# Optimization experiments

Hardware: AMD Instinct MI355X
Metric: run time of the kernel (lower is better)

## Reference

```python
import jax, jax.numpy as jnp
import numpy as np
import math

# Poincare ball, curvature c=1 (fixed, requires_grad=False in source)
C = 1.0
SQC = math.sqrt(C)
EPS = 1e-15
BALL_EPS = 1e-5  # projection margin onto the open ball


def _beta(n):
    # B(n/2, 1/2) -- beta-concatenation scale from HNN++ (Shimizu et al.)
    return math.exp(math.lgamma(n / 2.0) + math.lgamma(0.5) - math.lgamma((n + 1) / 2.0))


def _project(x, axis):
    max_norm = (1.0 - BALL_EPS) / SQC
    n = jnp.linalg.norm(x, axis=axis, keepdims=True)
    return x * jnp.minimum(1.0, max_norm / jnp.maximum(n, EPS))


def _expmap0(v, axis):
    n = jnp.maximum(jnp.linalg.norm(v, axis=axis, keepdims=True), EPS)
    return _project(jnp.tanh(SQC * n) * v / (SQC * n), axis)


def _logmap0(x, axis):
    n = jnp.maximum(jnp.linalg.norm(x, axis=axis, keepdims=True), EPS)
    sn = jnp.minimum(SQC * n, 1.0 - 1e-7)
    return jnp.arctanh(sn) * x / (SQC * n)


def _hrelu(x, axis):
    # HReLU: relu in the tangent space at the origin
    return _expmap0(jax.nn.relu(_logmap0(x, axis)), axis)


def _poincare_fc(x, z, r):
    # Poincare fully-connected layer (HNN++): x [..., d_in], z [d_in, d_out], r [d_out]
    zn = jnp.maximum(jnp.linalg.norm(z, axis=0), EPS)        # [d_out]
    zu = z / zn                                               # unit columns
    cx2 = C * jnp.sum(x * x, axis=-1, keepdims=True)          # c*||x||^2
    drcr = 2.0 * SQC * r                                      # [d_out]
    # unidirectional Poincare MLR
    v = (2.0 * zn / SQC) * jnp.arcsinh(
        (2.0 * SQC * (x @ zu) * jnp.cosh(drcr) - (1.0 + cx2) * jnp.sinh(drcr))
        / jnp.maximum(1.0 - cx2, EPS)
    )
    # map generalized coordinates back onto the ball
    y = jnp.sinh(SQC * v) / SQC
    y = y / (1.0 + jnp.sqrt(1.0 + C * jnp.sum(y * y, axis=-1, keepdims=True)))
    return _project(y, -1)


def _hconv(x, z, r, k):
    # HConvolution2d: beta-concat unfold of kxk patches (man_dim = channels), then Poincare FC
    B, Cin, H, W = x.shape
    oh, ow = H - k + 1, W - k + 1
    v = _logmap0(x, axis=1) * (_beta(Cin * k * k) / _beta(Cin))
    # torch.F.unfold ordering: feature index = c*k*k + i*k + j
    patches = jnp.stack([v[:, :, i:i + oh, j:j + ow] for i in range(k) for j in range(k)], axis=2)
    p = patches.reshape(B, Cin * k * k, oh * ow)
    xp = _expmap0(p, axis=1).transpose(0, 2, 1)   # [B, L, Cin*k*k]
    out = _poincare_fc(xp, z, r)                  # [B, L, Cout]
    return out.transpose(0, 2, 1).reshape(B, -1, oh, ow)


def _hmaxpool2(x):
    # HMaxPool2d(kernel=2, stride=2): pick the patch element with max distance to origin
    # (distance is monotonic in the norm, so argmax over channel norm suffices)
    B, Cc, H, W = x.shape
    h, w = H // 2, W // 2
    xb = x.reshape(B, Cc, h, 2, w, 2).transpose(0, 2, 4, 1, 3, 5).reshape(B, h, w, Cc, 4)
    nb = jnp.sum(xb * xb, axis=3)                 # [B, h, w, 4] squared norms
    idx = jnp.argmax(nb, axis=-1)                 # [B, h, w]
    out = jnp.take_along_axis(xb, idx[..., None, None], axis=-1)[..., 0]  # [B, h, w, Cc]
    return out.transpose(0, 3, 1, 2)


def _hflatten(x):
    # ManifoldTensor.flatten(start_dim=1): beta-concatenation flatten (man_dim 1 -> last)
    B, Cin = x.shape[0], x.shape[1]
    n = x.shape[1] * x.shape[2] * x.shape[3]
    v = _logmap0(x, axis=1) * (_beta(n) / _beta(Cin))
    return _expmap0(v.reshape(B, n), axis=-1)


def setup_inputs() -> dict:
    key = jax.random.key(0)
    ks = jax.random.split(key, 12)
    B = 1024
    s = 0.05
    x = _expmap0(0.1 * jax.random.normal(ks[0], (B, 3, 32, 32), jnp.float32), axis=1)
    return {
        "x": x,
        "z1": s * jax.random.normal(ks[1], (75, 6), jnp.float32),    # 3*5*5 -> 6
        "b1": s * jax.random.normal(ks[2], (6,), jnp.float32),
        "z2": s * jax.random.normal(ks[3], (150, 16), jnp.float32),  # 6*5*5 -> 16
        "b2": s * jax.random.normal(ks[4], (16,), jnp.float32),
        "zf1": s * jax.random.normal(ks[5], (400, 120), jnp.float32),
        "bf1": s * jax.random.normal(ks[6], (120,), jnp.float32),
        "zf2": s * jax.random.normal(ks[7], (120, 84), jnp.float32),
        "bf2": s * jax.random.normal(ks[8], (84,), jnp.float32),
        "zf3": s * jax.random.normal(ks[9], (84, 10), jnp.float32),
        "bf3": s * jax.random.normal(ks[10], (10,), jnp.float32),
    }


def reference(x, z1, b1, z2, b2, zf1, bf1, zf2, bf2, zf3, bf3):
    h = _hmaxpool2(_hrelu(_hconv(x, z1, b1, 5), axis=1))    # [B,6,14,14]
    h = _hmaxpool2(_hrelu(_hconv(h, z2, b2, 5), axis=1))    # [B,16,5,5]
    h = _hflatten(h)                                         # [B,400]
    h = _hrelu(_poincare_fc(h, zf1, bf1), axis=-1)
    h = _hrelu(_poincare_fc(h, zf2, bf2), axis=-1)
    return _poincare_fc(h, zf3, bf3)                         # [B,10]
```

## Files before the change

kernel.cpp:

```cpp
#include <hip/hip_runtime.h>
#include <cmath>

#define EPSF 1e-15f
#define MAXN 0.99999f

#define OFF_ZU1  0
#define OFF_P1   512
#define OFF_ZU2  576
#define OFF_P2   3072
#define OFF_PF1  3200
#define OFF_PF2  3584
#define OFF_PF3  3904
#define OFF_BUF1 4096
#define OFF_BUF3 (OFF_BUF1 + 1204224)

__device__ __forceinline__ float fast_tanh_pos(float x) {
    float e = __expf(-2.0f * x);
    return (1.0f - e) / (1.0f + e);
}
__device__ __forceinline__ float fast_atanh01(float x) {
    return 0.5f * __logf((1.0f + x) / (1.0f - x));
}
__device__ __forceinline__ float sinh_k_asinh(float t, float k) {
    float at = fabsf(t);
    float lq = __logf(at + sqrtf(fmaf(at, at, 1.0f)));
    float p = __expf(k * lq);
    float r = 0.5f * (p - 1.0f / p);
    return t < 0.f ? -r : r;
}

__device__ __forceinline__ float wave_reduce_sum(float s) {
#pragma unroll
    for (int d = 1; d < 64; d <<= 1) s += __shfl_xor(s, d);
    return s;
}

__global__ __launch_bounds__(64) void prep_kernel(
        const float* __restrict__ z1, const float* __restrict__ r1,
        const float* __restrict__ z2, const float* __restrict__ r2,
        const float* __restrict__ zf1, const float* __restrict__ rf1,
        const float* __restrict__ zf2, const float* __restrict__ rf2,
        const float* __restrict__ zf3, const float* __restrict__ rf3,
        float* __restrict__ ws) {
    int blk = blockIdx.x, lane = threadIdx.x;
    const float* z; const float* r; int Din, Dout, o;
    float* zu = nullptr; float* par;
    if (blk < 6)        { z = z1;  r = r1;  Din = 75;  Dout = 6;   o = blk;       zu = ws + OFF_ZU1; par = ws + OFF_P1; }
    else if (blk < 22)  { z = z2;  r = r2;  Din = 150; Dout = 16;  o = blk - 6;   zu = ws + OFF_ZU2; par = ws + OFF_P2; }
    else if (blk < 142) { z = zf1; r = rf1; Din = 400; Dout = 120; o = blk - 22;  par = ws + OFF_PF1; }
    else if (blk < 226) { z = zf2; r = rf2; Din = 120; Dout = 84;  o = blk - 142; par = ws + OFF_PF2; }
    else                { z = zf3; r = rf3; Din = 84;  Dout = 10;  o = blk - 226; par = ws + OFF_PF3; }
    float s = 0.f;
    for (int f = lane; f < Din; f += 64) { float w = z[f * Dout + o]; s += w * w; }
    s = wave_reduce_sum(s);
    float zn = fmaxf(sqrtf(s), EPSF);
    if (lane == 0) {
        par[o] = zn;
        par[Dout + o]     = coshf(2.0f * r[o]);
        par[2 * Dout + o] = sinhf(2.0f * r[o]);
    }
    if (zu)
        for (int f = lane; f < Din; f += 64) zu[f * Dout + o] = z[f * Dout + o] / zn;
}

template<int N>
__device__ __forceinline__ float chain_fast(float (&a)[N], float n2,
        const float (&zn)[N], const float (&ch)[N], const float (&sh)[N]) {
    float nn = fmaxf(sqrtf(n2), EPSF);
    float t = fast_tanh_pos(nn);
    float s = t / nn * fminf(1.0f, MAXN / fmaxf(t, EPSF));
    float cx2 = (s * s) * n2;
    float denom = fmaxf(1.0f - cx2, EPSF);
    float ys2 = 0.f;
#pragma unroll
    for (int o = 0; o < N; o++) {
        float arg = (2.0f * (s * a[o]) * ch[o] - (1.0f + cx2) * sh[o]) / denom;
        float yy = sinh_k_asinh(arg, 2.0f * zn[o]);
        a[o] = yy; ys2 += yy * yy;
    }
    float dnm = 1.0f + sqrtf(1.0f + ys2);
    float ny2 = ys2 / (dnm * dnm);
    float ny = fmaxf(sqrtf(ny2), EPSF);
    float pf = fminf(1.0f, MAXN / ny);
    float sc = pf / dnm;
    float n2b = pf * pf * ny2;
    float nb = fmaxf(sqrtf(n2b), EPSF);
    float fb = fast_atanh01(fminf(nb, 1.0f - 1e-7f)) / nb;
    float m2 = 0.f;
#pragma unroll
    for (int o = 0; o < N; o++) { float uu = fmaxf(fb * sc * a[o], 0.f); a[o] = uu; m2 += uu * uu; }
    float m = fmaxf(sqrtf(m2), EPSF);
    float tm = fast_tanh_pos(m);
    float g = tm / m * fminf(1.0f, MAXN / fmaxf(tm, EPSF));
#pragma unroll
    for (int o = 0; o < N; o++) a[o] *= g;
    return g * g * m2;
}

__global__ __launch_bounds__(256) void conv1_kernel(const float* __restrict__ x,
        const float* __restrict__ ws, float* __restrict__ out, float ratio) {
    __shared__ float xv[6144];
    __shared__ float us[2][4704];
    __shared__ float hn2s[2][784];
    int b0 = blockIdx.x * 2, tid = threadIdx.x;
    const float* zug  = ws + OFF_ZU1;
    const float* parg = ws + OFF_P1;
    for (int i = tid; i < 6144; i += 256) xv[i] = x[(size_t)b0 * 3072 + i];
    __syncthreads();
    for (int p = tid; p < 2048; p += 256) {
        int img = p >> 10, pix = p & 1023;
        float* xb = xv + img * 3072;
        float a0 = xb[pix], a1 = xb[pix + 1024], a2 = xb[pix + 2048];
        float n2 = a0 * a0 + a1 * a1 + a2 * a2;
        float nn = fmaxf(sqrtf(n2), EPSF);
        float f = fast_atanh01(fminf(nn, 1.0f - 1e-7f)) / nn * ratio;
        xb[pix] = a0 * f; xb[pix + 1024] = a1 * f; xb[pix + 2048] = a2 * f;
    }
    __syncthreads();
    if (tid < 224) {
        int img = tid / 112, u = tid % 112;
        int row = u >> 2, ox0 = (u & 3) * 7;
        const float* xb = xv + img * 3072;
        float acc[7][6];
        float n2[7];
#pragma unroll
        for (int w = 0; w < 7; w++) {
            n2[w] = 0.f;
#pragma unroll
            for (int o = 0; o < 6; o++) acc[w][o] = 0.f;
        }
#pragma unroll 1
        for (int c = 0; c < 3; c++) {
#pragma unroll 1
            for (int i = 0; i < 5; i++) {
                const float* rp = xb + c * 1024 + (row + i) * 32 + ox0;
                float xr[11];
#pragma unroll
                for (int k = 0; k < 11; k++) xr[k] = rp[k];
                const float* zp = zug + (c * 5 + i) * 30;
#pragma unroll
                for (int j = 0; j < 5; j++) {
                    float zw[6];
#pragma unroll
                    for (int o = 0; o < 6; o++) zw[o] = zp[j * 6 + o];
#pragma unroll
                    for (int w = 0; w < 7; w++) {
                        float v = xr[j + w];
                        n2[w] = fmaf(v, v, n2[w]);
#pragma unroll
                        for (int o = 0; o < 6; o++) acc[w][o] = fmaf(v, zw[o], acc[w][o]);
                    }
                }
            }
        }
        float zn[6], chv[6], shv[6];
#pragma unroll
        for (int o = 0; o < 6; o++) { zn[o] = parg[o]; chv[o] = parg[6 + o]; shv[o] = parg[12 + o]; }
#pragma unroll
        for (int w = 0; w < 7; w++) {
            float hn2 = chain_fast<6>(acc[w], n2[w], zn, chv, shv);
            int wx = row * 28 + ox0 + w;
#pragma unroll
            for (int o = 0; o < 6; o++) us[img][wx * 6 + o] = acc[w][o];
            hn2s[img][wx] = hn2;
        }
    }
    __syncthreads();
    for (int t = tid; t < 392; t += 256) {
        int img = t / 196, cell = t % 196;
        int ph = cell / 14, pw = cell % 14;
        float bv = -1.f; int bw = 0;
#pragma unroll
        for (int dy = 0; dy < 2; dy++)
#pragma unroll
        for (int dx = 0; dx < 2; dx++) {
            int w = (2 * ph + dy) * 28 + (2 * pw + dx);
            float v = hn2s[img][w];
            if (v > bv) { bv = v; bw = w; }
        }
        float* op = out + (size_t)(b0 + img) * 1176 + cell;
#pragma unroll
        for (int o = 0; o < 6; o++) op[o * 196] = us[img][bw * 6 + o];
    }
}

__global__ __launch_bounds__(256) void conv2_kernel(const float* __restrict__ in,
        const float* __restrict__ ws, float* __restrict__ out,
        float ratio2, float ratio3) {
    __shared__ float xv[4][1176];
    __shared__ float us[4][1600];
    __shared__ float hn2s[4][100];
    __shared__ int   win[4][25];
    __shared__ float fcs[4][25];
    __shared__ float gsh[4];
    int b0 = blockIdx.x * 4, tid = threadIdx.x;
    const float* zug  = ws + OFF_ZU2;
    const float* parg = ws + OFF_P2;
    for (int i = tid; i < 4704; i += 256) xv[0][i] = in[(size_t)b0 * 1176 + i];
    __syncthreads();
    for (int t = tid; t < 784; t += 256) {
        int img = t / 196, p = t % 196;
        float* xb = xv[img];
        float a[6]; float n2 = 0.f;
#pragma unroll
        for (int c = 0; c < 6; c++) { float v = xb[c * 196 + p]; a[c] = v; n2 += v * v; }
        float nn = fmaxf(sqrtf(n2), EPSF);
        float f = fast_atanh01(fminf(nn, 1.0f - 1e-7f)) / nn * ratio2;
#pragma unroll
        for (int c = 0; c < 6; c++) xb[c * 196 + p] = a[c] * f;
    }
    __syncthreads();
    if (tid < 160) {
        int img = tid / 40, r = tid % 40;
        int row = r >> 2, q = r & 3;
        int ox0 = (q & 1) * 5, h = q >> 1;
        const float* xb = xv[img];
        float acc[5][8];
        float n2[5];
#pragma unroll
        for (int w = 0; w < 5; w++) {
            n2[w] = 0.f;
#pragma unroll
            for (int o = 0; o < 8; o++) acc[w][o] = 0.f;
        }
#pragma unroll 1
        for (int c = 0; c < 6; c++) {
#pragma unroll 1
            for (int i = 0; i < 5; i++) {
                const float* rp = xb + c * 196 + (row + i) * 14 + ox0;
                float xr[9];
#pragma unroll
                for (int k = 0; k < 9; k++) xr[k] = rp[k];
                const float* zp = zug + (c * 5 + i) * 80 + 8 * h;
#pragma unroll
                for (int j = 0; j < 5; j++) {
                    float zw[8];
#pragma unroll
                    for (int o = 0; o < 8; o++) zw[o] = zp[j * 16 + o];
#pragma unroll
                    for (int w = 0; w < 5; w++) {
                        float v = xr[j + w];
                        n2[w] = fmaf(v, v, n2[w]);
#pragma unroll
                        for (int o = 0; o < 8; o++) acc[w][o] = fmaf(v, zw[o], acc[w][o]);
                    }
                }
            }
        }
        float zn[8], chv[8], shv[8];
#pragma unroll
        for (int o = 0; o < 8; o++) {
            zn[o] = parg[8 * h + o];
            chv[o] = parg[16 + 8 * h + o];
            shv[o] = parg[32 + 8 * h + o];
        }
#pragma unroll
        for (int w = 0; w < 5; w++) {
            float nn = fmaxf(sqrtf(n2[w]), EPSF);
            float t = fast_tanh_pos(nn);
            float s = t / nn * fminf(1.0f, MAXN / fmaxf(t, EPSF));
            float cx2 = (s * s) * n2[w];
            float denom = fmaxf(1.0f - cx2, EPSF);
            float y[8];
            float ys2h = 0.f;
#pragma unroll
            for (int o = 0; o < 8; o++) {
                float arg = (2.0f * (s * acc[w][o]) * chv[o] - (1.0f + cx2) * shv[o]) / denom;
                float yy = sinh_k_asinh(arg, 2.0f * zn[o]);
                y[o] = yy; ys2h += yy * yy;
            }
            float ys2 = ys2h + __shfl_xor(ys2h, 2);
            float dnm = 1.0f + sqrtf(1.0f + ys2);
            float ny2 = ys2 / (dnm * dnm);
            float ny = fmaxf(sqrtf(ny2), EPSF);
            float pf = fminf(1.0f, MAXN / ny);
            float sc = pf / dnm;
            float n2b = pf * pf * ny2;
            float nb = fmaxf(sqrtf(n2b), EPSF);
            float fb = fast_atanh01(fminf(nb, 1.0f - 1e-7f)) / nb;
            float m2h = 0.f;
#pragma unroll
            for (int o = 0; o < 8; o++) { float uu = fmaxf(fb * sc * y[o], 0.f); y[o] = uu; m2h += uu * uu; }
            float m2 = m2h + __shfl_xor(m2h, 2);
            float m = fmaxf(sqrtf(m2), EPSF);
            float tm = fast_tanh_pos(m);
            float g = tm / m * fminf(1.0f, MAXN / fmaxf(tm, EPSF));
            int wx = row * 10 + ox0 + w;
#pragma unroll
            for (int o = 0; o < 8; o++) us[img][wx * 16 + 8 * h + o] = g * y[o];
            if (h == 0) hn2s[img][wx] = g * g * m2;
        }
    }
    __syncthreads();
    {
        int img = tid >> 6, l = tid & 63;
        float part = 0.f;
        if (l < 25) {
            int ph = l / 5, pw = l % 5;
            float bv = -1.f; int bw = 0;
#pragma unroll
            for (int dy = 0; dy < 2; dy++)
#pragma unroll
            for (int dx = 0; dx < 2; dx++) {
                int w = (2 * ph + dy) * 10 + (2 * pw + dx);
                float v = hn2s[img][w];
                if (v > bv) { bv = v; bw = w; }
            }
            win[img][l] = bw;
            float h2 = hn2s[img][bw];
            float nn = fmaxf(sqrtf(h2), EPSF);
            float f = fast_atanh01(fminf(nn, 1.0f - 1e-7f)) / nn * ratio3;
            fcs[img][l] = f;
            part = f * f * h2;
        }
#pragma unroll
        for (int d = 1; d < 32; d <<= 1) part += __shfl_xor(part, d);
        if (l == 0) {
            float nn = fmaxf(sqrtf(part), EPSF);
            float t = fast_tanh_pos(nn);
            gsh[img] = t / nn * fminf(1.0f, MAXN / fmaxf(t, EPSF));
        }
    }
    __syncthreads();
    for (int i = tid; i < 1600; i += 256) {
        int img = i / 400, k = i % 400, o = k / 25, cell = k % 25;
        out[(size_t)(b0 + img) * 400 + k] =
            gsh[img] * fcs[img][cell] * us[img][win[img][cell] * 16 + o];
    }
}

template<int DIN, int DOUT, bool RELU>
__device__ __forceinline__ float fc_layer_wave(int lane, const float* __restrict__ xr,
        float cx2, const float* __restrict__ z, const float* __restrict__ par,
        float* __restrict__ dst) {
    int o0 = lane, o1 = lane + 64;
    bool v0 = o0 < DOUT, v1 = o1 < DOUT;
    int c0 = v0 ? o0 : 0, c1 = v1 ? o1 : 0;
    float d0 = 0.f, d1 = 0.f;
    for (int f = 0; f < DIN; f++) {
        float v = xr[f];
        d0 = fmaf(v, z[f * DOUT + c0], d0);
        if (DOUT > 64) d1 = fmaf(v, z[f * DOUT + c1], d1);
    }
    float denom = fmaxf(1.0f - cx2, EPSF);
    float zn0 = par[c0], ch0 = par[DOUT + c0], sh0 = par[2 * DOUT + c0];
    float arg0 = (2.0f * (d0 / zn0) * ch0 - (1.0f + cx2) * sh0) / denom;
    float y0 = sinh_k_asinh(arg0, 2.0f * zn0);
    float y1 = 0.f;
    if (DOUT > 64) {
        float zn1 = par[c1], ch1 = par[DOUT + c1], sh1 = par[2 * DOUT + c1];
        float arg1 = (2.0f * (d1 / zn1) * ch1 - (1.0f + cx2) * sh1) / denom;
        y1 = sinh_k_asinh(arg1, 2.0f * zn1);
    }
    float ys2 = wave_reduce_sum((v0 ? y0 * y0 : 0.f) + (v1 ? y1 * y1 : 0.f));
    float dnm = 1.0f + sqrtf(1.0f + ys2);
    float ny2 = ys2 / (dnm * dnm);
    float ny = fmaxf(sqrtf(ny2), EPSF);
    float pf = fminf(1.0f, MAXN / ny);
    float sc = pf / dnm;
    if (!RELU) {
        if (v0) dst[o0] = sc * y0;
        if (DOUT > 64 && v1) dst[o1] = sc * y1;
        return pf * pf * ny2;
    }
    float n2b = pf * pf * ny2;
    float nb = fmaxf(sqrtf(n2b), EPSF);
    float fb = fast_atanh01(fminf(nb, 1.0f - 1e-7f)) / nb;
    float u0 = fmaxf(fb * sc * y0, 0.f);
    float u1 = fmaxf(fb * sc * y1, 0.f);
    float m2 = wave_reduce_sum((v0 ? u0 * u0 : 0.f) + (v1 ? u1 * u1 : 0.f));
    float m = fmaxf(sqrtf(m2), EPSF);
    float tm = fast_tanh_pos(m);
    float g = tm / m * fminf(1.0f, MAXN / fmaxf(tm, EPSF));
    if (v0) dst[o0] = g * u0;
    if (DOUT > 64 && v1) dst[o1] = g * u1;
    return g * g * m2;
}

__global__ __launch_bounds__(256) void fc_stack_kernel(const float* __restrict__ in,
        const float* __restrict__ zf1, const float* __restrict__ zf2,
        const float* __restrict__ zf3, const float* __restrict__ ws,
        float* __restrict__ out) {
    __shared__ float xs[4][400];
    __shared__ float h1[4][120];
    __shared__ float h2[4][84];
    int wid = threadIdx.x >> 6, lane = threadIdx.x & 63;
    int b = blockIdx.x * 4 + wid;
    float* xr = xs[wid];
    float p = 0.f;
    for (int j = lane; j < 400; j += 64) { float v = in[(size_t)b * 400 + j]; xr[j] = v; p += v * v; }
    float cx2 = wave_reduce_sum(p);
    __syncthreads();
    float cx2b = fc_layer_wave<400, 120, true >(lane, xr,      cx2,  zf1, ws + OFF_PF1, h1[wid]);
    __syncthreads();
    float cx2c = fc_layer_wave<120, 84,  true >(lane, h1[wid], cx2b, zf2, ws + OFF_PF2, h2[wid]);
    __syncthreads();
    fc_layer_wave<84, 10, false>(lane, h2[wid], cx2c, zf3, ws + OFF_PF3, out + (size_t)b * 10);
}

static double beta_fn(double n) {
    return exp(lgamma(n / 2.0) + lgamma(0.5) - lgamma((n + 1) / 2.0));
}

extern "C" void kernel_launch(void* const* d_in, const int* in_sizes, int n_in,
                              void* d_out, int out_size, void* d_ws, size_t ws_size,
                              hipStream_t stream) {
    (void)in_sizes; (void)n_in; (void)out_size; (void)ws_size;
    const float* x   = (const float*)d_in[0];
    const float* z1  = (const float*)d_in[1];
    const float* b1  = (const float*)d_in[2];
    const float* z2  = (const float*)d_in[3];
    const float* b2  = (const float*)d_in[4];
    const float* zf1 = (const float*)d_in[5];
    const float* bf1 = (const float*)d_in[6];
    const float* zf2 = (const float*)d_in[7];
    const float* bf2 = (const float*)d_in[8];
    const float* zf3 = (const float*)d_in[9];
    const float* bf3 = (const float*)d_in[10];
    float* out = (float*)d_out;
    float* ws  = (float*)d_ws;

    const float ratio1 = (float)(beta_fn(75.0)  / beta_fn(3.0));
    const float ratio2 = (float)(beta_fn(150.0) / beta_fn(6.0));
    const float ratio3 = (float)(beta_fn(400.0) / beta_fn(6.0) * beta_fn(6.0) / beta_fn(16.0));

    float* buf1 = ws + OFF_BUF1;
    float* buf3 = ws + OFF_BUF3;

    prep_kernel<<<236, 64, 0, stream>>>(z1, b1, z2, b2, zf1, bf1, zf2, bf2, zf3, bf3, ws);
    conv1_kernel<<<512, 256, 0, stream>>>(x, ws, buf1, ratio1);
    conv2_kernel<<<256, 256, 0, stream>>>(buf1, ws, buf3, ratio2, ratio3);
    fc_stack_kernel<<<256, 256, 0, stream>>>(buf3, zf1, zf2, zf3, ws, out);
}
```

Before: 174.8 us.

## Restructure conv kernels to compute per-pool-cell windows and fuse maxpool in registers

```diff
diff --git a/kernel.cpp b/kernel.cpp
--- a/kernel.cpp
+++ b/kernel.cpp
@@ -99,177 +99,172 @@
 
 __global__ __launch_bounds__(256) void conv1_kernel(const float* __restrict__ x,
         const float* __restrict__ ws, float* __restrict__ out, float ratio) {
-    __shared__ float xv[6144];
-    __shared__ float us[2][4704];
-    __shared__ float hn2s[2][784];
-    int b0 = blockIdx.x * 2, tid = threadIdx.x;
+    __shared__ float xv[3168];
+    int b = blockIdx.x, tid = threadIdx.x;
     const float* zug  = ws + OFF_ZU1;
     const float* parg = ws + OFF_P1;
-    for (int i = tid; i < 6144; i += 256) xv[i] = x[(size_t)b0 * 3072 + i];
-    __syncthreads();
-    for (int p = tid; p < 2048; p += 256) {
-        int img = p >> 10, pix = p & 1023;
-        float* xb = xv + img * 3072;
-        float a0 = xb[pix], a1 = xb[pix + 1024], a2 = xb[pix + 2048];
+    for (int i = tid; i < 3072; i += 256) {
+        int c = i >> 10, rem = i & 1023;
+        xv[c * 1056 + (rem >> 5) * 33 + (rem & 31)] = x[(size_t)b * 3072 + i];
+    }
+    __syncthreads();
+    for (int p = tid; p < 1024; p += 256) {
+        int base = (p >> 5) * 33 + (p & 31);
+        float a0 = xv[base], a1 = xv[1056 + base], a2 = xv[2112 + base];
         float n2 = a0 * a0 + a1 * a1 + a2 * a2;
         float nn = fmaxf(sqrtf(n2), EPSF);
         float f = fast_atanh01(fminf(nn, 1.0f - 1e-7f)) / nn * ratio;
-        xb[pix] = a0 * f; xb[pix + 1024] = a1 * f; xb[pix + 2048] = a2 * f;
-    }
-    __syncthreads();
-    if (tid < 224) {
-        int img = tid / 112, u = tid % 112;
-        int row = u >> 2, ox0 = (u & 3) * 7;
-        const float* xb = xv + img * 3072;
-        float acc[7][6];
-        float n2[7];
-#pragma unroll
-        for (int w = 0; w < 7; w++) {
-            n2[w] = 0.f;
-#pragma unroll
-            for (int o = 0; o < 6; o++) acc[w][o] = 0.f;
-        }
+        xv[base] = a0 * f; xv[1056 + base] = a1 * f; xv[2112 + base] = a2 * f;
+    }
+    __syncthreads();
+    if (tid >= 196) return;
+    int ph = tid / 14, pw = tid % 14;
+    int base0 = (2 * ph) * 33 + 2 * pw;
+    float acc[4][6], n2w[4];
+#pragma unroll
+    for (int wi = 0; wi < 4; wi++) {
+        n2w[wi] = 0.f;
+#pragma unroll
+        for (int o = 0; o < 6; o++) acc[wi][o] = 0.f;
+    }
 #pragma unroll 1
-        for (int c = 0; c < 3; c++) {
+    for (int c = 0; c < 3; c++) {
+        float px[6][6];
+#pragma unroll
+        for (int r = 0; r < 6; r++)
+#pragma unroll
+        for (int j = 0; j < 6; j++)
+            px[r][j] = xv[c * 1056 + base0 + r * 33 + j];
+#pragma unroll
+        for (int fi = 0; fi < 5; fi++) {
+            const float* zp = zug + (c * 5 + fi) * 30;
+#pragma unroll
+            for (int fj = 0; fj < 5; fj++) {
+                float zw[6];
+#pragma unroll
+                for (int o = 0; o < 6; o++) zw[o] = zp[fj * 6 + o];
+#pragma unroll
+                for (int dy = 0; dy < 2; dy++)
+#pragma unroll
+                for (int dx = 0; dx < 2; dx++) {
+                    float v = px[fi + dy][fj + dx];
+                    int wi = dy * 2 + dx;
+                    n2w[wi] = fmaf(v, v, n2w[wi]);
+#pragma unroll
+                    for (int o = 0; o < 6; o++) acc[wi][o] = fmaf(v, zw[o], acc[wi][o]);
+                }
+            }
+        }
+    }
+    float zn[6], chv[6], shv[6];
+#pragma unroll
+    for (int o = 0; o < 6; o++) { zn[o] = parg[o]; chv[o] = parg[6 + o]; shv[o] = parg[12 + o]; }
+    float best[6]; float bestn = -1.f;
+#pragma unroll
+    for (int wi = 0; wi < 4; wi++) {
+        float hn2 = chain_fast<6>(acc[wi], n2w[wi], zn, chv, shv);
+        if (hn2 > bestn) {
+            bestn = hn2;
+#pragma unroll
+            for (int o = 0; o < 6; o++) best[o] = acc[wi][o];
+        }
+    }
+    float* op = out + (size_t)b * 1176 + tid;
+#pragma unroll
+    for (int o = 0; o < 6; o++) op[o * 196] = best[o];
+}
+
+__global__ __launch_bounds__(128) void conv2_kernel(const float* __restrict__ in,
+        const float* __restrict__ ws, float* __restrict__ out,
+        float ratio2, float ratio3) {
+    __shared__ float xv[2522];
+    int b0 = blockIdx.x * 2, tid = threadIdx.x;
+    const float* zug  = ws + OFF_ZU2;
+    const float* parg = ws + OFF_P2;
+    for (int i = tid; i < 2352; i += 128) {
+        int img = i / 1176, rem = i % 1176;
+        int c = rem / 196, pix = rem % 196;
+        xv[img * 1261 + c * 210 + (pix / 14) * 15 + pix % 14] = in[(size_t)b0 * 1176 + i];
+    }
+    __syncthreads();
+    for (int t = tid; t < 392; t += 128) {
+        int img = t / 196, pix = t % 196;
+        int base = img * 1261 + (pix / 14) * 15 + pix % 14;
+        float a[6]; float n2 = 0.f;
+#pragma unroll
+        for (int c = 0; c < 6; c++) { float v = xv[base + c * 210]; a[c] = v; n2 += v * v; }
+        float nn = fmaxf(sqrtf(n2), EPSF);
+        float f = fast_atanh01(fminf(nn, 1.0f - 1e-7f)) / nn * ratio2;
+#pragma unroll
+        for (int c = 0; c < 6; c++) xv[base + c * 210] = a[c] * f;
+    }
+    __syncthreads();
+    int img = tid >> 6, l = tid & 63;
+    int cell = l >> 1, h = l & 1;
+    bool act = cell < 25;
+    float best[8];
+    float bestn = -1.f;
+    float fcell = 0.f, part = 0.f;
+    if (act) {
+        int base0 = img * 1261 + (2 * (cell / 5)) * 15 + 2 * (cell % 5);
+        float acc[4][8], n2w[4];
+#pragma unroll
+        for (int wi = 0; wi < 4; wi++) {
+            n2w[wi] = 0.f;
+#pragma unroll
+            for (int o = 0; o < 8; o++) acc[wi][o] = 0.f;
+        }
 #pragma unroll 1
-            for (int i = 0; i < 5; i++) {
-                const float* rp = xb + c * 1024 + (row + i) * 32 + ox0;
-                float xr[11];
-#pragma unroll
-                for (int k = 0; k < 11; k++) xr[k] = rp[k];
-                const float* zp = zug + (c * 5 + i) * 30;
-#pragma unroll
-                for (int j = 0; j < 5; j++) {
-                    float zw[6];
-#pragma unroll
-                    for (int o = 0; o < 6; o++) zw[o] = zp[j * 6 + o];
-#pragma unroll
-                    for (int w = 0; w < 7; w++) {
-                        float v = xr[j + w];
-                        n2[w] = fmaf(v, v, n2[w]);
-#pragma unroll
-                        for (int o = 0; o < 6; o++) acc[w][o] = fmaf(v, zw[o], acc[w][o]);
+        for (int c = 0; c < 6; c++) {
+            float px[6][6];
+#pragma unroll
+            for (int r = 0; r < 6; r++)
+#pragma unroll
+            for (int j = 0; j < 6; j++)
+                px[r][j] = xv[base0 + c * 210 + r * 15 + j];
+#pragma unroll
+            for (int fi = 0; fi < 5; fi++) {
+                const float* zp = zug + (c * 5 + fi) * 80 + 8 * h;
+#pragma unroll
+                for (int fj = 0; fj < 5; fj++) {
+                    float zw[8];
+#pragma unroll
+                    for (int o = 0; o < 8; o++) zw[o] = zp[fj * 16 + o];
+#pragma unroll
+                    for (int dy = 0; dy < 2; dy++)
+#pragma unroll
+                    for (int dx = 0; dx < 2; dx++) {
+                        float v = px[fi + dy][fj + dx];
+                        int wi = dy * 2 + dx;
+                        n2w[wi] = fmaf(v, v, n2w[wi]);
+#pragma unroll
+                        for (int o = 0; o < 8; o++) acc[wi][o] = fmaf(v, zw[o], acc[wi][o]);
                     }
                 }
             }
         }
-        float zn[6], chv[6], shv[6];
-#pragma unroll
-        for (int o = 0; o < 6; o++) { zn[o] = parg[o]; chv[o] = parg[6 + o]; shv[o] = parg[12 + o]; }
-#pragma unroll
-        for (int w = 0; w < 7; w++) {
-            float hn2 = chain_fast<6>(acc[w], n2[w], zn, chv, shv);
-            int wx = row * 28 + ox0 + w;
-#pragma unroll
-            for (int o = 0; o < 6; o++) us[img][wx * 6 + o] = acc[w][o];
-            hn2s[img][wx] = hn2;
-        }
-    }
-    __syncthreads();
-    for (int t = tid; t < 392; t += 256) {
-        int img = t / 196, cell = t % 196;
-        int ph = cell / 14, pw = cell % 14;
-        float bv = -1.f; int bw = 0;
-#pragma unroll
-        for (int dy = 0; dy < 2; dy++)
-#pragma unroll
-        for (int dx = 0; dx < 2; dx++) {
-            int w = (2 * ph + dy) * 28 + (2 * pw + dx);
-            float v = hn2s[img][w];
-            if (v > bv) { bv = v; bw = w; }
-        }
-        float* op = out + (size_t)(b0 + img) * 1176 + cell;
-#pragma unroll
-        for (int o = 0; o < 6; o++) op[o * 196] = us[img][bw * 6 + o];
-    }
-}
-
-__global__ __launch_bounds__(256) void conv2_kernel(const float* __restrict__ in,
-        const float* __restrict__ ws, float* __restrict__ out,
-        float ratio2, float ratio3) {
-    __shared__ float xv[4][1176];
-    __shared__ float us[4][1600];
-    __shared__ float hn2s[4][100];
-    __shared__ int   win[4][25];
-    __shared__ float fcs[4][25];
-    __shared__ float gsh[4];
-    int b0 = blockIdx.x * 4, tid = threadIdx.x;
-    const float* zug  = ws + OFF_ZU2;
-    const float* parg = ws + OFF_P2;
-    for (int i = tid; i < 4704; i += 256) xv[0][i] = in[(size_t)b0 * 1176 + i];
-    __syncthreads();
-    for (int t = tid; t < 784; t += 256) {
-        int img = t / 196, p = t % 196;
-        float* xb = xv[img];
-        float a[6]; float n2 = 0.f;
-#pragma unroll
-        for (int c = 0; c < 6; c++) { float v = xb[c * 196 + p]; a[c] = v; n2 += v * v; }
-        float nn = fmaxf(sqrtf(n2), EPSF);
-        float f = fast_atanh01(fminf(nn, 1.0f - 1e-7f)) / nn * ratio2;
-#pragma unroll
-        for (int c = 0; c < 6; c++) xb[c * 196 + p] = a[c] * f;
-    }
-    __syncthreads();
-    if (tid < 160) {
-        int img = tid / 40, r = tid % 40;
-        int row = r >> 2, q = r & 3;
-        int ox0 = (q & 1) * 5, h = q >> 1;
-        const float* xb = xv[img];
-        float acc[5][8];
-        float n2[5];
-#pragma unroll
-        for (int w = 0; w < 5; w++) {
-            n2[w] = 0.f;
-#pragma unroll
-            for (int o = 0; o < 8; o++) acc[w][o] = 0.f;
-        }
-#pragma unroll 1
-        for (int c = 0; c < 6; c++) {
-#pragma unroll 1
-            for (int i = 0; i < 5; i++) {
-                const float* rp = xb + c * 196 + (row + i) * 14 + ox0;
-                float xr[9];
-#pragma unroll
-                for (int k = 0; k < 9; k++) xr[k] = rp[k];
-                const float* zp = zug + (c * 5 + i) * 80 + 8 * h;
-#pragma unroll
-                for (int j = 0; j < 5; j++) {
-                    float zw[8];
-#pragma unroll
-                    for (int o = 0; o < 8; o++) zw[o] = zp[j * 16 + o];
-#pragma unroll
-                    for (int w = 0; w < 5; w++) {
-                        float v = xr[j + w];
-                        n2[w] = fmaf(v, v, n2[w]);
-#pragma unroll
-                        for (int o = 0; o < 8; o++) acc[w][o] = fmaf(v, zw[o], acc[w][o]);
-                    }
-                }
-            }
-        }
         float zn[8], chv[8], shv[8];
 #pragma unroll
         for (int o = 0; o < 8; o++) {
-            zn[o] = parg[8 * h + o];
+            zn[o]  = parg[8 * h + o];
             chv[o] = parg[16 + 8 * h + o];
             shv[o] = parg[32 + 8 * h + o];
         }
 #pragma unroll
-        for (int w = 0; w < 5; w++) {
-            float nn = fmaxf(sqrtf(n2[w]), EPSF);
+        for (int wi = 0; wi < 4; wi++) {
+            float nn = fmaxf(sqrtf(n2w[wi]), EPSF);
             float t = fast_tanh_pos(nn);
             float s = t / nn * fminf(1.0f, MAXN / fmaxf(t, EPSF));
-            float cx2 = (s * s) * n2[w];
+            float cx2 = (s * s) * n2w[wi];
             float denom = fmaxf(1.0f - cx2, EPSF);
-            float y[8];
             float ys2h = 0.f;
 #pragma unroll
             for (int o = 0; o < 8; o++) {
-                float arg = (2.0f * (s * acc[w][o]) * chv[o] - (1.0f + cx2) * shv[o]) / denom;
+                float arg = (2.0f * (s * acc[wi][o]) * chv[o] - (1.0f + cx2) * shv[o]) / denom;
                 float yy = sinh_k_asinh(arg, 2.0f * zn[o]);
-                y[o] = yy; ys2h += yy * yy;
+                acc[wi][o] = yy; ys2h += yy * yy;
             }
-            float ys2 = ys2h + __shfl_xor(ys2h, 2);
+            float ys2 = ys2h + __shfl_xor(ys2h, 1);
             float dnm = 1.0f + sqrtf(1.0f + ys2);
             float ny2 = ys2 / (dnm * dnm);
             float ny = fmaxf(sqrtf(ny2), EPSF);
@@ -280,53 +275,44 @@
             float fb = fast_atanh01(fminf(nb, 1.0f - 1e-7f)) / nb;
             float m2h = 0.f;
 #pragma unroll
-            for (int o = 0; o < 8; o++) { float uu = fmaxf(fb * sc * y[o], 0.f); y[o] = uu; m2h += uu * uu; }
-            float m2 = m2h + __shfl_xor(m2h, 2);
+            for (int o = 0; o < 8; o++) { float uu = fmaxf(fb * sc * acc[wi][o], 0.f); acc[wi][o] = uu; m2h += uu * uu; }
+            float m2 = m2h + __shfl_xor(m2h, 1);
             float m = fmaxf(sqrtf(m2), EPSF);
             float tm = fast_tanh_pos(m);
             float g = tm / m * fminf(1.0f, MAXN / fmaxf(tm, EPSF));
-            int wx = row * 10 + ox0 + w;
-#pragma unroll
-            for (int o = 0; o < 8; o++) us[img][wx * 16 + 8 * h + o] = g * y[o];
-            if (h == 0) hn2s[img][wx] = g * g * m2;
-        }
-    }
-    __syncthreads();
-    {
-        int img = tid >> 6, l = tid & 63;
-        float part = 0.f;
-        if (l < 25) {
-            int ph = l / 5, pw = l % 5;
-            float bv = -1.f; int bw = 0;
-#pragma unroll
-            for (int dy = 0; dy < 2; dy++)
-#pragma unroll
-            for (int dx = 0; dx < 2; dx++) {
-                int w = (2 * ph + dy) * 10 + (2 * pw + dx);
-                float v = hn2s[img][w];
-                if (v > bv) { bv = v; bw = w; }
+            float hn2 = g * g * m2;
+            if (hn2 > bestn) {
+                bestn = hn2;
+#pragma unroll
+                for (int o = 0; o < 8; o++) best[o] = g * acc[wi][o];
             }
-            win[img][l] = bw;
-            float h2 = hn2s[img][bw];
-            float nn = fmaxf(sqrtf(h2), EPSF);
-            float f = fast_atanh01(fminf(nn, 1.0f - 1e-7f)) / nn * ratio3;
-            fcs[img][l] = f;
-            part = f * f * h2;
-        }
-#pragma unroll
-        for (int d = 1; d < 32; d <<= 1) part += __shfl_xor(part, d);
-        if (l == 0) {
-            float nn = fmaxf(sqrtf(part), EPSF);
-            float t = fast_tanh_pos(nn);
-            gsh[img] = t / nn * fminf(1.0f, MAXN / fmaxf(t, EPSF));
-        }
-    }
-    __syncthreads();
-    for (int i = tid; i < 1600; i += 256) {
-        int img = i / 400, k = i % 400, o = k / 25, cell = k % 25;
-        out[(size_t)(b0 + img) * 400 + k] =
-            gsh[img] * fcs[img][cell] * us[img][win[img][cell] * 16 + o];
-    }
+        }
+        float nn = fmaxf(sqrtf(bestn), EPSF);
+        fcell = fast_atanh01(fminf(nn, 1.0f - 1e-7f)) / nn * ratio3;
+        if (h == 0) part = fcell * fcell * bestn;
+    }
+    float s = wave_reduce_sum(part);
+    float nn = fmaxf(sqrtf(s), EPSF);
+    float t = fast_tanh_pos(nn);
+    float g = t / nn * fminf(1.0f, MAXN / fmaxf(t, EPSF));
+    if (act) {
+        float* op = out + (size_t)(b0 + img) * 400 + cell;
+#pragma unroll
+        for (int o = 0; o < 8; o++) op[(8 * h + o) * 25] = g * fcell * best[o];
+    }
+}
+
+template<int DIN, int DOUT>
+__device__ __forceinline__ float dot_col(const float* __restrict__ xr,
+        const float* __restrict__ z, int col) {
+    float a0 = 0.f, a1 = 0.f, a2 = 0.f, a3 = 0.f;
+    for (int f = 0; f < DIN; f += 4) {
+        a0 = fmaf(xr[f],     z[(f)     * DOUT + col], a0);
+        a1 = fmaf(xr[f + 1], z[(f + 1) * DOUT + col], a1);
+        a2 = fmaf(xr[f + 2], z[(f + 2) * DOUT + col], a2);
+        a3 = fmaf(xr[f + 3], z[(f + 3) * DOUT + col], a3);
+    }
+    return (a0 + a1) + (a2 + a3);
 }
 
 template<int DIN, int DOUT, bool RELU>
@@ -336,12 +322,8 @@
     int o0 = lane, o1 = lane + 64;
     bool v0 = o0 < DOUT, v1 = o1 < DOUT;
     int c0 = v0 ? o0 : 0, c1 = v1 ? o1 : 0;
-    float d0 = 0.f, d1 = 0.f;
-    for (int f = 0; f < DIN; f++) {
-        float v = xr[f];
-        d0 = fmaf(v, z[f * DOUT + c0], d0);
-        if (DOUT > 64) d1 = fmaf(v, z[f * DOUT + c1], d1);
-    }
+    float d0 = dot_col<DIN, DOUT>(xr, z, c0);
+    float d1 = (DOUT > 64) ? dot_col<DIN, DOUT>(xr, z, c1) : 0.f;
     float denom = fmaxf(1.0f - cx2, EPSF);
     float zn0 = par[c0], ch0 = par[DOUT + c0], sh0 = par[2 * DOUT + c0];
     float arg0 = (2.0f * (d0 / zn0) * ch0 - (1.0f + cx2) * sh0) / denom;
@@ -422,13 +404,13 @@
 
     const float ratio1 = (float)(beta_fn(75.0)  / beta_fn(3.0));
     const float ratio2 = (float)(beta_fn(150.0) / beta_fn(6.0));
-    const float ratio3 = (float)(beta_fn(400.0) / beta_fn(6.0) * beta_fn(6.0) / beta_fn(16.0));
+    const float ratio3 = (float)(beta_fn(400.0) / beta_fn(16.0));
 
     float* buf1 = ws + OFF_BUF1;
     float* buf3 = ws + OFF_BUF3;
 
     prep_kernel<<<236, 64, 0, stream>>>(z1, b1, z2, b2, zf1, bf1, zf2, bf2, zf3, bf3, ws);
-    conv1_kernel<<<512, 256, 0, stream>>>(x, ws, buf1, ratio1);
-    conv2_kernel<<<256, 256, 0, stream>>>(buf1, ws, buf3, ratio2, ratio3);
+    conv1_kernel<<<1024, 256, 0, stream>>>(x, ws, buf1, ratio1);
+    conv2_kernel<<<512, 128, 0, stream>>>(buf1, ws, buf3, ratio2, ratio3);
     fc_stack_kernel<<<256, 256, 0, stream>>>(buf3, zf1, zf2, zf3, ws, out);
 }
```

Result: slower. 182.9 us (+4.6%).
